# Kernel optimization log

Measured on AMD Instinct MI355X. Metric: run time of the kernel, lower is better.

Reference implementation:

```python
import jax, jax.numpy as jnp
import numpy as np

D_MODEL = 1024
NUM_HEADS = 16
HEAD_DIM = D_MODEL // NUM_HEADS


def setup_inputs() -> dict:
    key = jax.random.key(0)
    k1, k2, k3 = jax.random.split(key, 3)
    B, T = 4, 2048
    x = jax.random.normal(k1, (B, T, D_MODEL), dtype=jnp.float32)
    # nn.Linear weights: out = x @ W.T; store torch-layout [out_features, in_features]
    w_qkv = jax.random.normal(k2, (3 * D_MODEL, D_MODEL), dtype=jnp.float32) * (D_MODEL ** -0.5)
    w_proj = jax.random.normal(k3, (D_MODEL, D_MODEL), dtype=jnp.float32) * (D_MODEL ** -0.5)
    return {"x": x, "w_qkv": w_qkv, "w_proj": w_proj}


def reference(x, w_qkv, w_proj):
    B, T, C = x.shape
    H, Dh = NUM_HEADS, HEAD_DIM
    qkv = jnp.einsum('btc,fc->btf', x, w_qkv)          # [B,T,3C]
    q, k, v = jnp.split(qkv, 3, axis=2)
    # [B,T,C] -> [B,H,T,Dh]
    q = q.reshape(B, T, H, Dh).transpose(0, 2, 1, 3)
    k = k.reshape(B, T, H, Dh).transpose(0, 2, 1, 3)
    v = v.reshape(B, T, H, Dh).transpose(0, 2, 1, 3)
    scale = Dh ** -0.5
    att = jnp.einsum('bhqd,bhkd->bhqk', q, k) * scale  # [B,H,T,T]
    causal = jnp.tril(jnp.ones((T, T), dtype=bool))
    att = jnp.where(causal, att, -jnp.inf)
    att = jax.nn.softmax(att, axis=-1)
    y = jnp.einsum('bhqk,bhkd->bhqd', att, v)          # [B,H,T,Dh]
    y = y.transpose(0, 2, 1, 3).reshape(B, T, C)
    return jnp.einsum('btc,oc->bto', y, w_proj)
```

## Files before the change

kernel.cpp:

```cpp
#include <hip/hip_runtime.h>
#include <stdint.h>
#include <math.h>

typedef __bf16 bf16;
typedef __bf16 bf16x4 __attribute__((ext_vector_type(4)));
typedef __bf16 bf16x8 __attribute__((ext_vector_type(8)));
typedef float f32x4 __attribute__((ext_vector_type(4)));

#define MFMA16(a, b, c) __builtin_amdgcn_mfma_f32_16x16x32_bf16((a), (b), (c), 0, 0, 0)

typedef __attribute__((address_space(1))) void* as1v;
typedef __attribute__((address_space(3))) void* as3v;

__device__ __forceinline__ void async_ld16(const void* g, void* l) {
  __builtin_amdgcn_global_load_lds((as1v)(uintptr_t)g,
                                   (as3v)(unsigned int)(uintptr_t)l, 16, 0, 0);
}

__global__ __launch_bounds__(256) void cast3_k(const float* __restrict__ x,
                                               const float* __restrict__ wq,
                                               const float* __restrict__ wp,
                                               bf16* __restrict__ xb,
                                               bf16* __restrict__ wqb,
                                               bf16* __restrict__ wpb) {
  const long i = (long)blockIdx.x * 256 + threadIdx.x;
  const float4* src;
  bf16x4* dst;
  long off;
  if (i < 2097152L) {
    src = (const float4*)x;  dst = (bf16x4*)xb;  off = i;
  } else if (i < 2097152L + 786432L) {
    src = (const float4*)wq; dst = (bf16x4*)wqb; off = i - 2097152L;
  } else {
    src = (const float4*)wp; dst = (bf16x4*)wpb; off = i - 2097152L - 786432L;
  }
  float4 v = src[off];
  bf16x4 o;
  o[0] = (bf16)v.x; o[1] = (bf16)v.y; o[2] = (bf16)v.z; o[3] = (bf16)v.w;
  dst[off] = o;
}

__global__ __launch_bounds__(256, 2) void gemm_qkv(const bf16* __restrict__ A,
                                                   const bf16* __restrict__ Bm,
                                                   bf16* __restrict__ qb,
                                                   bf16* __restrict__ kb,
                                                   bf16* __restrict__ vth) {
  __shared__ bf16 As[256 * 64];
  __shared__ bf16 Bs[128 * 64];
  const int tid  = threadIdx.x;
  const int lane = tid & 63;
  const int wv   = tid >> 6;
  const int lr   = lane & 15;
  const int quad = lane >> 4;
  const long m0 = (long)blockIdx.y * 256;
  const long n0 = (long)blockIdx.x * 128;

  const int srow = lane >> 3;
  const int scg  = (lane & 7) ^ srow;
  const int swz  = lr & 7;

  const f32x4 fz = {0.f, 0.f, 0.f, 0.f};
  f32x4 acc[4][8];
#pragma unroll
  for (int i = 0; i < 4; ++i)
#pragma unroll
    for (int j = 0; j < 8; ++j) acc[i][j] = fz;

  for (int k0 = 0; k0 < 1024; k0 += 64) {
    __syncthreads();
#pragma unroll
    for (int i = 0; i < 8; ++i) {
      const int rb = wv * 64 + i * 8;
      async_ld16(&A[(m0 + rb + srow) * 1024 + k0 + scg * 8], &As[rb * 64]);
    }
#pragma unroll
    for (int i = 0; i < 4; ++i) {
      const int rb = wv * 32 + i * 8;
      async_ld16(&Bm[(n0 + rb + srow) * 1024 + k0 + scg * 8], &Bs[rb * 64]);
    }
    __syncthreads();

#pragma unroll
    for (int ds = 0; ds < 2; ++ds) {
      const int slot = ((ds << 2) + quad) ^ swz;
      bf16x8 af[4], bfr[8];
#pragma unroll
      for (int mi = 0; mi < 4; ++mi)
        af[mi] = *(const bf16x8*)&As[(wv * 64 + mi * 16 + lr) * 64 + slot * 8];
#pragma unroll
      for (int ni = 0; ni < 8; ++ni)
        bfr[ni] = *(const bf16x8*)&Bs[(ni * 16 + lr) * 64 + slot * 8];
#pragma unroll
      for (int mi = 0; mi < 4; ++mi)
#pragma unroll
        for (int ni = 0; ni < 8; ++ni)
          acc[mi][ni] = MFMA16(af[mi], bfr[ni], acc[mi][ni]);
    }
  }

  const int bx = blockIdx.x;
  if (bx < 8) {
    const float kS = 0.18033688f;
#pragma unroll
    for (int mi = 0; mi < 4; ++mi) {
      const long row = m0 + wv * 64 + mi * 16 + quad * 4;
#pragma unroll
      for (int ni = 0; ni < 8; ++ni) {
        const long col = n0 + ni * 16 + lr;
#pragma unroll
        for (int r = 0; r < 4; ++r) qb[(row + r) * 1024 + col] = (bf16)(acc[mi][ni][r] * kS);
      }
    }
  } else if (bx < 16) {
#pragma unroll
    for (int mi = 0; mi < 4; ++mi) {
      const long row = m0 + wv * 64 + mi * 16 + quad * 4;
#pragma unroll
      for (int ni = 0; ni < 8; ++ni) {
        const long col = n0 + ni * 16 + lr - 1024;
#pragma unroll
        for (int r = 0; r < 4; ++r) kb[(row + r) * 1024 + col] = (bf16)(acc[mi][ni][r]);
      }
    }
  } else {
#pragma unroll
    for (int mi = 0; mi < 4; ++mi) {
      const long row = m0 + wv * 64 + mi * 16 + quad * 4;
      const long b = row >> 11;
      const long t = row & 2047;
#pragma unroll
      for (int ni = 0; ni < 8; ++ni) {
        const long vcol = n0 + ni * 16 + lr - 2048;
        const long h = vcol >> 6, d = vcol & 63;
        bf16x4 pk;
#pragma unroll
        for (int r = 0; r < 4; ++r) pk[r] = (bf16)(acc[mi][ni][r]);
        *(bf16x4*)&vth[(((b << 4) + h) * 64 + d) * 2048 + t] = pk;
      }
    }
  }
}

__global__ __launch_bounds__(128, 2) void gemm_proj(const bf16* __restrict__ A,
                                                    const bf16* __restrict__ Bm,
                                                    float* __restrict__ C) {
  __shared__ bf16 As[128 * 64];
  __shared__ bf16 Bs[128 * 64];
  const int tid  = threadIdx.x;
  const int lane = tid & 63;
  const int wv   = tid >> 6;
  const int lr   = lane & 15;
  const int quad = lane >> 4;
  const long m0 = (long)blockIdx.y * 128;
  const long n0 = (long)blockIdx.x * 128;

  const int srow = lane >> 3;
  const int scg  = (lane & 7) ^ srow;
  const int swz  = lr & 7;

  const f32x4 fz = {0.f, 0.f, 0.f, 0.f};
  f32x4 acc[4][8];
#pragma unroll
  for (int i = 0; i < 4; ++i)
#pragma unroll
    for (int j = 0; j < 8; ++j) acc[i][j] = fz;

  for (int k0 = 0; k0 < 1024; k0 += 64) {
    __syncthreads();
#pragma unroll
    for (int i = 0; i < 8; ++i) {
      const int rb = wv * 64 + i * 8;
      async_ld16(&A[(m0 + rb + srow) * 1024 + k0 + scg * 8], &As[rb * 64]);
      async_ld16(&Bm[(n0 + rb + srow) * 1024 + k0 + scg * 8], &Bs[rb * 64]);
    }
    __syncthreads();

#pragma unroll
    for (int ds = 0; ds < 2; ++ds) {
      const int slot = ((ds << 2) + quad) ^ swz;
      bf16x8 af[4], bfr[8];
#pragma unroll
      for (int mi = 0; mi < 4; ++mi)
        af[mi] = *(const bf16x8*)&As[(wv * 64 + mi * 16 + lr) * 64 + slot * 8];
#pragma unroll
      for (int ni = 0; ni < 8; ++ni)
        bfr[ni] = *(const bf16x8*)&Bs[(ni * 16 + lr) * 64 + slot * 8];
#pragma unroll
      for (int mi = 0; mi < 4; ++mi)
#pragma unroll
        for (int ni = 0; ni < 8; ++ni)
          acc[mi][ni] = MFMA16(af[mi], bfr[ni], acc[mi][ni]);
    }
  }

#pragma unroll
  for (int mi = 0; mi < 4; ++mi) {
    const long row = m0 + wv * 64 + mi * 16 + quad * 4;
#pragma unroll
    for (int ni = 0; ni < 8; ++ni) {
      const long col = n0 + ni * 16 + lr;
#pragma unroll
      for (int r = 0; r < 4; ++r) C[(row + r) * 1024 + col] = acc[mi][ni][r];
    }
  }
}

__global__ __launch_bounds__(256, 2) void flash_attn5(const bf16* __restrict__ q,
                                                      const bf16* __restrict__ k,
                                                      const bf16* __restrict__ vth,
                                                      bf16* __restrict__ y) {
  __shared__ bf16 Ks[2][64 * 64];
  __shared__ bf16 Vt[64 * 64];
  __shared__ bf16 Ps[4][32 * 72];
  const int tid  = threadIdx.x;
  const int lane = tid & 63;
  const int wv   = tid >> 6;
  const int lr   = lane & 15;
  const int quad = lane >> 4;
  const int p  = blockIdx.x;
  const int bh = blockIdx.y;
  const int b = bh >> 4, h = bh & 15;
  const bf16* qp = q + ((size_t)b * 2048) * 1024 + h * 64;
  const bf16* kp = k + ((size_t)b * 2048) * 1024 + h * 64;
  const bf16* vp = vth + (size_t)bh * 64 * 2048;
  bf16* yp = y + ((size_t)b * 2048) * 1024 + h * 64;

  const int stg_row = lane >> 3;
  const int stg_cg  = (lane & 7) ^ stg_row;
  const int swz     = lr & 7;

  bf16x8 ones;
#pragma unroll
  for (int j = 0; j < 8; ++j) ones[j] = (bf16)1.0f;
  const f32x4 fz = {0.f, 0.f, 0.f, 0.f};

  for (int half = 0; half < 2; ++half) {
    const int qt = half ? p : 15 - p;
    const int q0 = qt * 128;
    const int kb_max = 2 * qt + 1;
    const int kmax_w = 2 * qt + (wv >> 1);

    bf16x8 qf[2][2];
#pragma unroll
    for (int nq = 0; nq < 2; ++nq) {
      const int qrow = q0 + wv * 32 + nq * 16 + lr;
#pragma unroll
      for (int ds = 0; ds < 2; ++ds)
        qf[nq][ds] = *(const bf16x8*)(qp + (size_t)qrow * 1024 + ds * 32 + quad * 8);
    }

    f32x4 o[2][4];
    f32x4 lacc[2];
#pragma unroll
    for (int nq = 0; nq < 2; ++nq) {
      lacc[nq] = fz;
#pragma unroll
      for (int nf = 0; nf < 4; ++nf) o[nq][nf] = fz;
    }

    __syncthreads();
#pragma unroll
    for (int i = 0; i < 2; ++i) {
      const int r = i * 32 + wv * 8 + stg_row;
      async_ld16(kp + (size_t)r * 1024 + stg_cg * 8, &Ks[0][(i * 32 + wv * 8) * 64]);
    }

    for (int kt = 0; kt <= kb_max; ++kt) {
      const int k0 = kt * 64;
      const int cb = kt & 1;
      __syncthreads();
      if (kt < kb_max) {
#pragma unroll
        for (int i = 0; i < 2; ++i) {
          const int r = i * 32 + wv * 8 + stg_row;
          async_ld16(kp + (size_t)(k0 + 64 + r) * 1024 + stg_cg * 8,
                     &Ks[cb ^ 1][(i * 32 + wv * 8) * 64]);
        }
      }
#pragma unroll
      for (int i = 0; i < 2; ++i) {
        const int r = i * 32 + wv * 8 + stg_row;
        async_ld16(vp + (size_t)r * 2048 + k0 + stg_cg * 8, &Vt[(i * 32 + wv * 8) * 64]);
      }

      const bool act = (kt <= kmax_w);
      bf16x8 ap[2][2];
      if (act) {
        f32x4 s[2][4];
#pragma unroll
        for (int nq = 0; nq < 2; ++nq)
#pragma unroll
          for (int mi = 0; mi < 4; ++mi) s[nq][mi] = fz;
#pragma unroll
        for (int ds = 0; ds < 2; ++ds)
#pragma unroll
          for (int mi = 0; mi < 4; ++mi) {
            const bf16x8 ak =
                *(const bf16x8*)&Ks[cb][(mi * 16 + lr) * 64 + (((ds << 2) + quad) ^ swz) * 8];
            s[0][mi] = MFMA16(ak, qf[0][ds], s[0][mi]);
            s[1][mi] = MFMA16(ak, qf[1][ds], s[1][mi]);
          }

        if (kt < kmax_w) {
#pragma unroll
          for (int nq = 0; nq < 2; ++nq) {
            const int qloc = nq * 16 + lr;
#pragma unroll
            for (int mi = 0; mi < 4; ++mi) {
              bf16x4 pb;
#pragma unroll
              for (int r = 0; r < 4; ++r) pb[r] = (bf16)__builtin_amdgcn_exp2f(s[nq][mi][r]);
              *(bf16x4*)&Ps[wv][qloc * 72 + mi * 16 + quad * 4] = pb;
            }
          }
        } else {
          const int kofs = k0 - q0 - wv * 32;
#pragma unroll
          for (int nq = 0; nq < 2; ++nq) {
            const int qloc = nq * 16 + lr;
#pragma unroll
            for (int mi = 0; mi < 4; ++mi) {
              bf16x4 pb;
#pragma unroll
              for (int r = 0; r < 4; ++r) {
                float pv = __builtin_amdgcn_exp2f(s[nq][mi][r]);
                if (mi * 16 + quad * 4 + r + kofs > qloc) pv = 0.0f;
                pb[r] = (bf16)pv;
              }
              *(bf16x4*)&Ps[wv][qloc * 72 + mi * 16 + quad * 4] = pb;
            }
          }
        }
#pragma unroll
        for (int ks = 0; ks < 2; ++ks) {
          ap[0][ks] = *(const bf16x8*)&Ps[wv][(lr) * 72 + ks * 32 + quad * 8];
          ap[1][ks] = *(const bf16x8*)&Ps[wv][(16 + lr) * 72 + ks * 32 + quad * 8];
        }
      }

      __syncthreads();

      if (act) {
#pragma unroll
        for (int ks = 0; ks < 2; ++ks) {
          lacc[0] = MFMA16(ap[0][ks], ones, lacc[0]);
          lacc[1] = MFMA16(ap[1][ks], ones, lacc[1]);
#pragma unroll
          for (int nf = 0; nf < 4; ++nf) {
            const bf16x8 bv =
                *(const bf16x8*)&Vt[(nf * 16 + lr) * 64 + (((ks << 2) + quad) ^ swz) * 8];
            o[0][nf] = MFMA16(ap[0][ks], bv, o[0][nf]);
            o[1][nf] = MFMA16(ap[1][ks], bv, o[1][nf]);
          }
        }
      }
    }

#pragma unroll
    for (int nq = 0; nq < 2; ++nq)
#pragma unroll
      for (int r = 0; r < 4; ++r) {
        const float inv = __builtin_amdgcn_rcpf(lacc[nq][r]);
        const int t = q0 + wv * 32 + nq * 16 + quad * 4 + r;
#pragma unroll
        for (int nf = 0; nf < 4; ++nf)
          yp[(size_t)t * 1024 + nf * 16 + lr] = (bf16)(o[nq][nf][r] * inv);
      }
  }
}

extern "C" void kernel_launch(void* const* d_in, const int* in_sizes, int n_in,
                              void* d_out, int out_size, void* d_ws, size_t ws_size,
                              hipStream_t stream) {
  const float* x      = (const float*)d_in[0];
  const float* w_qkv  = (const float*)d_in[1];
  const float* w_proj = (const float*)d_in[2];
  float* out = (float*)d_out;
  char* ws = (char*)d_ws;

  bf16* xb   = (bf16*)(ws);
  bf16* wqkb = (bf16*)(ws + (16ull << 20));
  bf16* wpb  = (bf16*)(ws + (22ull << 20));
  bf16* qb   = (bf16*)(ws + (24ull << 20));
  bf16* kbuf = (bf16*)(ws + (40ull << 20));
  bf16* vth  = (bf16*)(ws + (56ull << 20));
  bf16* yb   = (bf16*)(ws + (72ull << 20));

  cast3_k<<<dim3(12288), 256, 0, stream>>>(x, w_qkv, w_proj, xb, wqkb, wpb);
  gemm_qkv<<<dim3(24, 32), 256, 0, stream>>>(xb, wqkb, qb, kbuf, vth);
  flash_attn5<<<dim3(8, 64), 256, 0, stream>>>(qb, kbuf, vth, yb);
  gemm_proj<<<dim3(8, 64), 128, 0, stream>>>(yb, wpb, out);
}
```

Measured before the change: 232.5 us.

## Double-buffer QKV GEMM LDS and retile to 256x192 with 8 waves

The QKV projection GEMM now uses two LDS buffers, so the async global-to-LDS load of the next k-tile is issued before computing on the current one, with one barrier per iteration instead of two. The block tile grows from 256x128 to 256x192 with 512 threads arranged as a 4x2 wave grid, giving 512 blocks instead of 768, and the epilogue picks the Q, K or V destination per column instead of per block. LDS use rises to about 112 KB per block, so only one block may fit per CU despite the launch bound of 2, and the grid becomes two full waves of blocks over the CUs.

```diff
diff --git a/kernel.cpp b/kernel.cpp
--- a/kernel.cpp
+++ b/kernel.cpp
@@ -40,102 +40,98 @@
   dst[off] = o;
 }
 
-__global__ __launch_bounds__(256, 2) void gemm_qkv(const bf16* __restrict__ A,
+__global__ __launch_bounds__(512, 2) void gemm_qkv(const bf16* __restrict__ A,
                                                    const bf16* __restrict__ Bm,
                                                    bf16* __restrict__ qb,
                                                    bf16* __restrict__ kb,
                                                    bf16* __restrict__ vth) {
-  __shared__ bf16 As[256 * 64];
-  __shared__ bf16 Bs[128 * 64];
+  __shared__ bf16 As[2][256 * 64];
+  __shared__ bf16 Bs[2][192 * 64];
   const int tid  = threadIdx.x;
   const int lane = tid & 63;
   const int wv   = tid >> 6;
+  const int wm   = wv >> 1;
+  const int wn   = wv & 1;
   const int lr   = lane & 15;
   const int quad = lane >> 4;
   const long m0 = (long)blockIdx.y * 256;
-  const long n0 = (long)blockIdx.x * 128;
+  const long n0 = (long)blockIdx.x * 192;
 
   const int srow = lane >> 3;
   const int scg  = (lane & 7) ^ srow;
   const int swz  = lr & 7;
 
   const f32x4 fz = {0.f, 0.f, 0.f, 0.f};
-  f32x4 acc[4][8];
+  f32x4 acc[4][6];
 #pragma unroll
   for (int i = 0; i < 4; ++i)
 #pragma unroll
-    for (int j = 0; j < 8; ++j) acc[i][j] = fz;
-
-  for (int k0 = 0; k0 < 1024; k0 += 64) {
-    __syncthreads();
-#pragma unroll
-    for (int i = 0; i < 8; ++i) {
-      const int rb = wv * 64 + i * 8;
-      async_ld16(&A[(m0 + rb + srow) * 1024 + k0 + scg * 8], &As[rb * 64]);
-    }
-#pragma unroll
-    for (int i = 0; i < 4; ++i) {
-      const int rb = wv * 32 + i * 8;
-      async_ld16(&Bm[(n0 + rb + srow) * 1024 + k0 + scg * 8], &Bs[rb * 64]);
-    }
-    __syncthreads();
-
+    for (int j = 0; j < 6; ++j) acc[i][j] = fz;
+
+#define STAGE_QKV(kt, bufi)                                                        \
+  do {                                                                             \
+    const long kk = (long)(kt) * 64;                                               \
+    _Pragma("unroll") for (int i_ = 0; i_ < 4; ++i_)                               \
+        async_ld16(&A[(m0 + i_ * 64 + wv * 8 + srow) * 1024 + kk + scg * 8],       \
+                   &As[bufi][(i_ * 64 + wv * 8) * 64]);                            \
+    _Pragma("unroll") for (int i_ = 0; i_ < 3; ++i_)                               \
+        async_ld16(&Bm[(n0 + i_ * 64 + wv * 8 + srow) * 1024 + kk + scg * 8],      \
+                   &Bs[bufi][(i_ * 64 + wv * 8) * 64]);                            \
+  } while (0)
+
+  STAGE_QKV(0, 0);
+  __syncthreads();
+
+  for (int t = 0; t < 16; ++t) {
+    const int cur = t & 1;
+    if (t < 15) STAGE_QKV(t + 1, cur ^ 1);
+
+    bf16x8 af[2][4], bfr[2][6];
 #pragma unroll
     for (int ds = 0; ds < 2; ++ds) {
       const int slot = ((ds << 2) + quad) ^ swz;
-      bf16x8 af[4], bfr[8];
 #pragma unroll
       for (int mi = 0; mi < 4; ++mi)
-        af[mi] = *(const bf16x8*)&As[(wv * 64 + mi * 16 + lr) * 64 + slot * 8];
-#pragma unroll
-      for (int ni = 0; ni < 8; ++ni)
-        bfr[ni] = *(const bf16x8*)&Bs[(ni * 16 + lr) * 64 + slot * 8];
+        af[ds][mi] = *(const bf16x8*)&As[cur][(wm * 64 + mi * 16 + lr) * 64 + slot * 8];
+#pragma unroll
+      for (int ni = 0; ni < 6; ++ni)
+        bfr[ds][ni] = *(const bf16x8*)&Bs[cur][(wn * 96 + ni * 16 + lr) * 64 + slot * 8];
+    }
+#pragma unroll
+    for (int ds = 0; ds < 2; ++ds)
 #pragma unroll
       for (int mi = 0; mi < 4; ++mi)
 #pragma unroll
-        for (int ni = 0; ni < 8; ++ni)
-          acc[mi][ni] = MFMA16(af[mi], bfr[ni], acc[mi][ni]);
-    }
-  }
-
-  const int bx = blockIdx.x;
-  if (bx < 8) {
-    const float kS = 0.18033688f;
-#pragma unroll
-    for (int mi = 0; mi < 4; ++mi) {
-      const long row = m0 + wv * 64 + mi * 16 + quad * 4;
-#pragma unroll
-      for (int ni = 0; ni < 8; ++ni) {
-        const long col = n0 + ni * 16 + lr;
+        for (int ni = 0; ni < 6; ++ni)
+          acc[mi][ni] = MFMA16(af[ds][mi], bfr[ds][ni], acc[mi][ni]);
+
+    __syncthreads();
+  }
+#undef STAGE_QKV
+
+  const float kS = 0.18033688f;
+#pragma unroll
+  for (int mi = 0; mi < 4; ++mi) {
+    const long row = m0 + wm * 64 + mi * 16 + quad * 4;
+#pragma unroll
+    for (int ni = 0; ni < 6; ++ni) {
+      const long col = n0 + wn * 96 + ni * 16 + lr;
+      if (col < 1024) {
 #pragma unroll
         for (int r = 0; r < 4; ++r) qb[(row + r) * 1024 + col] = (bf16)(acc[mi][ni][r] * kS);
-      }
-    }
-  } else if (bx < 16) {
-#pragma unroll
-    for (int mi = 0; mi < 4; ++mi) {
-      const long row = m0 + wv * 64 + mi * 16 + quad * 4;
-#pragma unroll
-      for (int ni = 0; ni < 8; ++ni) {
-        const long col = n0 + ni * 16 + lr - 1024;
-#pragma unroll
-        for (int r = 0; r < 4; ++r) kb[(row + r) * 1024 + col] = (bf16)(acc[mi][ni][r]);
-      }
-    }
-  } else {
-#pragma unroll
-    for (int mi = 0; mi < 4; ++mi) {
-      const long row = m0 + wv * 64 + mi * 16 + quad * 4;
-      const long b = row >> 11;
-      const long t = row & 2047;
-#pragma unroll
-      for (int ni = 0; ni < 8; ++ni) {
-        const long vcol = n0 + ni * 16 + lr - 2048;
+      } else if (col < 2048) {
+        const long kc = col - 1024;
+#pragma unroll
+        for (int r = 0; r < 4; ++r) kb[(row + r) * 1024 + kc] = (bf16)(acc[mi][ni][r]);
+      } else {
+        const long vcol = col - 2048;
         const long h = vcol >> 6, d = vcol & 63;
+        const long b = row >> 11;
+        const long tt = row & 2047;
         bf16x4 pk;
 #pragma unroll
         for (int r = 0; r < 4; ++r) pk[r] = (bf16)(acc[mi][ni][r]);
-        *(bf16x4*)&vth[(((b << 4) + h) * 64 + d) * 2048 + t] = pk;
+        *(bf16x4*)&vth[(((b << 4) + h) * 64 + d) * 2048 + tt] = pk;
       }
     }
   }
@@ -387,7 +383,7 @@
   bf16* yb   = (bf16*)(ws + (72ull << 20));
 
   cast3_k<<<dim3(12288), 256, 0, stream>>>(x, w_qkv, w_proj, xb, wqkb, wpb);
-  gemm_qkv<<<dim3(24, 32), 256, 0, stream>>>(xb, wqkb, qb, kbuf, vth);
+  gemm_qkv<<<dim3(16, 32), 512, 0, stream>>>(xb, wqkb, qb, kbuf, vth);
   flash_attn5<<<dim3(8, 64), 256, 0, stream>>>(qb, kbuf, vth, yb);
   gemm_proj<<<dim3(8, 64), 128, 0, stream>>>(yb, wpb, out);
 }
```

After: 235.1 us. Within noise of the previous version (+1.1%).
